# Kernel optimization log

Hardware: AMD Instinct MI355X
Metric: run time of the kernel (lower is better)

## Reference

```python
import jax, jax.numpy as jnp
import numpy as np

SPHERE_C = 128
M0 = 5            # m_size[0] = lmax+1
M_ALL = 19        # sum(m_size) for lmax=4, mmax=2
NUM_COEFF = 25    # (lmax+1)^2
RESCALE = 16.0
EPS = 1e-6        # flax LayerNorm default


def _layer_norm(h, g, b):
    mu = jnp.mean(h, axis=-1, keepdims=True)
    var = jnp.var(h, axis=-1, keepdims=True)
    return (h - mu) * jax.lax.rsqrt(var + EPS) * g + b


def setup_inputs() -> dict:
    key = jax.random.key(0)
    ks = jax.random.split(key, 16)
    n_nodes, n_edges = 6250, 100000
    inp = {
        'x': jax.random.normal(ks[0], (n_nodes, NUM_COEFF, SPHERE_C), jnp.float32),
        'x_edge': jax.random.normal(ks[1], (n_edges, 128), jnp.float32),
        'edge_index': jax.random.randint(ks[2], (2, n_edges), 0, n_nodes),
        'wigner_inv': jax.random.normal(ks[3], (n_edges, NUM_COEFF, M_ALL), jnp.float32),
        'edge_envelope': jax.random.uniform(ks[4], (n_edges, 1, 1), jnp.float32),
        'node_offset': 0,
    }
    # Radial MLP params: channels [128, 128, 128, M0*SPHERE_C=640]
    def lin(k, fan_in, fan_out):
        return jax.random.normal(k, (fan_in, fan_out), jnp.float32) / np.sqrt(fan_in).astype(np.float32)
    inp['W1'] = lin(ks[5], 128, 128); inp['b1'] = jnp.zeros((128,), jnp.float32)
    inp['g1'] = jnp.ones((128,), jnp.float32); inp['be1'] = jnp.zeros((128,), jnp.float32)
    inp['W2'] = lin(ks[6], 128, 128); inp['b2'] = jnp.zeros((128,), jnp.float32)
    inp['g2'] = jnp.ones((128,), jnp.float32); inp['be2'] = jnp.zeros((128,), jnp.float32)
    inp['W3'] = lin(ks[7], 128, M0 * SPHERE_C); inp['b3'] = jnp.zeros((M0 * SPHERE_C,), jnp.float32)
    return inp


def reference(x, x_edge, edge_index, wigner_inv, edge_envelope, node_offset,
              W1, b1, g1, be1, W2, b2, g2, be2, W3, b3):
    # Radial MLP: (Linear -> LayerNorm -> SiLU) x2 -> Linear
    h = jax.nn.silu(_layer_norm(x_edge @ W1 + b1, g1, be1))
    h = jax.nn.silu(_layer_norm(h @ W2 + b2, g2, be2))
    h = h @ W3 + b3                                      # [E, M0*C]
    x_edge_m_0 = h.reshape(-1, M0, SPHERE_C)             # [E, M0, C]
    # Embedding is zero for m>0 coefficients, so rotate only the first M0 columns
    # of wigner_inv: equivalent to padding to M_ALL then full einsum.
    emb = jnp.einsum('njk,nkc->njc', wigner_inv[:, :, :M0], x_edge_m_0)  # [E, 25, C]
    emb = emb * edge_envelope
    tgt = edge_index[1] - node_offset
    x_update = jax.ops.segment_sum(emb, tgt, num_segments=x.shape[0])
    return x + x_update / RESCALE
```

## Files before the change

kernel.cpp:

```cpp
#include <hip/hip_runtime.h>
#include <hip/hip_bf16.h>

typedef __attribute__((ext_vector_type(8))) short short8;
typedef __attribute__((ext_vector_type(4))) float floatx4;

static __device__ inline unsigned short f2bf(float f) {
    unsigned u = __float_as_uint(f);
    unsigned r = (u + 0x7fffu + ((u >> 16) & 1u)) >> 16;
    return (unsigned short)r;
}

__global__ __launch_bounds__(256) void mlp12_kernel(
    const float* __restrict__ xe,
    const float* __restrict__ W1, const float* __restrict__ b1,
    const float* __restrict__ g1, const float* __restrict__ be1,
    const float* __restrict__ W2, const float* __restrict__ b2,
    const float* __restrict__ g2, const float* __restrict__ be2,
    unsigned short* __restrict__ h2b, int E)
{
    __shared__ float As[64 * 132];
    __shared__ float Bs[16 * 128];
    __shared__ float redS[64 * 16];
    __shared__ float redQ[64 * 16];
    __shared__ float mrow[64];
    __shared__ float rrow[64];

    int t  = threadIdx.x;
    int tx = t & 15;
    int ty = t >> 4;
    int e0 = blockIdx.x * 64;

    for (int idx = t; idx < 64 * 32; idx += 256) {
        int row = idx >> 5;
        int c4  = (idx & 31) * 4;
        float4 v = make_float4(0.f, 0.f, 0.f, 0.f);
        if (e0 + row < E) v = *(const float4*)(xe + (size_t)(e0 + row) * 128 + c4);
        *(float4*)&As[row * 132 + c4] = v;
    }

    const float* Wl = W1; const float* bl = b1; const float* gl = g1; const float* bel = be1;
    float acc[4][8];

    for (int layer = 0; layer < 2; layer++) {
        for (int r = 0; r < 4; r++)
            for (int i = 0; i < 8; i++) acc[r][i] = 0.f;

        for (int kk = 0; kk < 128; kk += 16) {
            __syncthreads();
            for (int idx = t; idx < 16 * 32; idx += 256) {
                int row = idx >> 5;
                int c4  = (idx & 31) * 4;
                *(float4*)&Bs[row * 128 + c4] = *(const float4*)(Wl + (size_t)(kk + row) * 128 + c4);
            }
            __syncthreads();
            for (int k4 = 0; k4 < 16; k4 += 4) {
                float b[4][8];
                #pragma unroll
                for (int kb = 0; kb < 4; kb++) {
                    float4 bv0 = *(float4*)&Bs[(k4 + kb) * 128 + tx * 8];
                    float4 bv1 = *(float4*)&Bs[(k4 + kb) * 128 + tx * 8 + 4];
                    b[kb][0] = bv0.x; b[kb][1] = bv0.y; b[kb][2] = bv0.z; b[kb][3] = bv0.w;
                    b[kb][4] = bv1.x; b[kb][5] = bv1.y; b[kb][6] = bv1.z; b[kb][7] = bv1.w;
                }
                #pragma unroll
                for (int r = 0; r < 4; r++) {
                    float4 a4 = *(float4*)&As[(ty * 4 + r) * 132 + kk + k4];
                    #pragma unroll
                    for (int i = 0; i < 8; i++)
                        acc[r][i] += a4.x * b[0][i] + a4.y * b[1][i]
                                   + a4.z * b[2][i] + a4.w * b[3][i];
                }
            }
        }

        float gg[8], bebe[8];
        for (int i = 0; i < 8; i++) {
            float bb = bl[tx * 8 + i];
            gg[i]    = gl[tx * 8 + i];
            bebe[i]  = bel[tx * 8 + i];
            for (int r = 0; r < 4; r++) acc[r][i] += bb;
        }
        for (int r = 0; r < 4; r++) {
            float s = 0.f, q = 0.f;
            for (int i = 0; i < 8; i++) { s += acc[r][i]; q += acc[r][i] * acc[r][i]; }
            redS[(ty * 4 + r) * 16 + tx] = s;
            redQ[(ty * 4 + r) * 16 + tx] = q;
        }
        __syncthreads();
        if (t < 64) {
            float s = 0.f, q = 0.f;
            for (int i = 0; i < 16; i++) { s += redS[t * 16 + i]; q += redQ[t * 16 + i]; }
            float mu  = s * (1.f / 128.f);
            float var = q * (1.f / 128.f) - mu * mu;
            mrow[t] = mu;
            rrow[t] = rsqrtf(var + 1e-6f);
        }
        __syncthreads();
        for (int r = 0; r < 4; r++) {
            int e_loc = ty * 4 + r;
            float mu = mrow[e_loc], rs = rrow[e_loc];
            for (int i = 0; i < 8; i++) {
                float v = (acc[r][i] - mu) * rs * gg[i] + bebe[i];
                acc[r][i] = v / (1.f + __expf(-v));
            }
        }
        if (layer == 0) {
            for (int r = 0; r < 4; r++) {
                int e_loc = ty * 4 + r;
                for (int i = 0; i < 8; i++) As[e_loc * 132 + tx * 8 + i] = acc[r][i];
            }
            __syncthreads();
            Wl = W2; bl = b2; gl = g2; bel = be2;
        } else {
            for (int r = 0; r < 4; r++) {
                int e = e0 + ty * 4 + r;
                if (e < E) {
                    unsigned p[4];
                    for (int i = 0; i < 4; i++)
                        p[i] = (unsigned)f2bf(acc[r][2 * i]) | ((unsigned)f2bf(acc[r][2 * i + 1]) << 16);
                    *(uint4*)(h2b + (size_t)e * 128 + tx * 8) = make_uint4(p[0], p[1], p[2], p[3]);
                }
            }
        }
    }
}

__global__ __launch_bounds__(256) void w3t_kernel(const float* __restrict__ W3,
                                                  unsigned short* __restrict__ W3bT)
{
    int idx = blockIdx.x * 256 + threadIdx.x;
    int n = idx >> 7, k = idx & 127;
    W3bT[idx] = f2bf(W3[(size_t)k * 640 + n]);
}

__global__ __launch_bounds__(256) void gemm3_mfma_kernel(
    const unsigned short* __restrict__ h2b, const unsigned short* __restrict__ W3bT,
    const float* __restrict__ b3, unsigned short* __restrict__ h3b, int E)
{
    __shared__ unsigned short As[64 * 136];

    int t    = threadIdx.x;
    int lane = t & 63;
    int w    = t >> 6;
    int mw   = w & 1, nw = w >> 1;
    int l15  = lane & 15, quad = lane >> 4;
    int e0   = blockIdx.x * 64;
    int n0   = blockIdx.y * 128;

    for (int p = 0; p < 4; p++) {
        int idx = p * 256 + t;
        int row = idx >> 4;
        int c16 = idx & 15;
        uint4 v = make_uint4(0, 0, 0, 0);
        if (e0 + row < E) v = *(const uint4*)(h2b + (size_t)(e0 + row) * 128 + c16 * 8);
        *(uint4*)&As[row * 136 + c16 * 8] = v;
    }

    short8 bfrag[4][4];
    {
        const unsigned short* bbase = W3bT + (size_t)(n0 + nw * 64) * 128;
        for (int ks = 0; ks < 4; ks++)
            for (int nf = 0; nf < 4; nf++)
                bfrag[ks][nf] = *(const short8*)(bbase + (size_t)(nf * 16 + l15) * 128 + ks * 32 + quad * 8);
    }

    floatx4 acc[2][4];
    for (int mf = 0; mf < 2; mf++)
        for (int nf = 0; nf < 4; nf++)
            acc[mf][nf] = (floatx4){0.f, 0.f, 0.f, 0.f};

    __syncthreads();

    for (int ks = 0; ks < 4; ks++) {
        short8 afrag[2];
        for (int mf = 0; mf < 2; mf++)
            afrag[mf] = *(const short8*)&As[(mw * 32 + mf * 16 + l15) * 136 + ks * 32 + quad * 8];
        for (int mf = 0; mf < 2; mf++)
            for (int nf = 0; nf < 4; nf++)
                acc[mf][nf] = __builtin_amdgcn_mfma_f32_16x16x32_bf16(
                    bfrag[ks][nf], afrag[mf], acc[mf][nf], 0, 0, 0);
    }

    for (int nf = 0; nf < 4; nf++) {
        float4 bias = *(const float4*)&b3[n0 + nw * 64 + nf * 16 + quad * 4];
        for (int mf = 0; mf < 2; mf++) {
            int m = e0 + mw * 32 + mf * 16 + l15;
            if (m < E) {
                floatx4 v = acc[mf][nf];
                unsigned lo = (unsigned)f2bf(v[0] + bias.x) | ((unsigned)f2bf(v[1] + bias.y) << 16);
                unsigned hi = (unsigned)f2bf(v[2] + bias.z) | ((unsigned)f2bf(v[3] + bias.w) << 16);
                *(uint2*)(h3b + (size_t)m * 640 + n0 + nw * 64 + nf * 16 + quad * 4) = make_uint2(lo, hi);
            }
        }
    }
}

__global__ void hist_kernel(const int* __restrict__ ei, const int* __restrict__ noff,
                            int* __restrict__ counts, int E)
{
    int i = blockIdx.x * blockDim.x + threadIdx.x;
    if (i < E) {
        int tgt = ei[E + i] - noff[0];
        atomicAdd(&counts[tgt], 1);
    }
}

__global__ __launch_bounds__(1024) void scan_kernel(const int* __restrict__ counts,
                                                    int* __restrict__ offsets,
                                                    int* __restrict__ cursor, int N)
{
    __shared__ int part[1024];
    int t = threadIdx.x;
    int per = (N + 1023) / 1024;
    int beg = t * per;
    int end = beg + per; if (end > N) end = N; if (beg > N) beg = N;
    int s = 0;
    for (int i = beg; i < end; i++) s += counts[i];
    part[t] = s;
    __syncthreads();
    for (int off = 1; off < 1024; off <<= 1) {
        int v = part[t];
        int u = (t >= off) ? part[t - off] : 0;
        __syncthreads();
        part[t] = v + u;
        __syncthreads();
    }
    int run = (t == 0) ? 0 : part[t - 1];
    for (int i = beg; i < end; i++) {
        offsets[i] = run;
        cursor[i]  = run;
        run += counts[i];
    }
    if (t == 1023) offsets[N] = part[1023];
}

__global__ void scatter_kernel(const int* __restrict__ ei, const int* __restrict__ noff,
                               int* __restrict__ cursor, int* __restrict__ edge_ids, int E)
{
    int i = blockIdx.x * blockDim.x + threadIdx.x;
    if (i < E) {
        int tgt = ei[E + i] - noff[0];
        int pos = atomicAdd(&cursor[tgt], 1);
        edge_ids[pos] = i;
    }
}

__global__ __launch_bounds__(256) void gather_kernel(
    const float* __restrict__ x, const unsigned short* __restrict__ h3b,
    const float* __restrict__ wig, const float* __restrict__ env,
    const int* __restrict__ offsets, const int* __restrict__ edge_ids,
    float* __restrict__ out, int N)
{
    __shared__ float sw[2][25 * 8];
    __shared__ float sh[2][640];
    __shared__ float sev[2];
    int n = blockIdx.x;
    int t = threadIdx.x;
    int c = t & 127;
    int half = t >> 7;
    int njj = half ? 12 : 13;
    float acc[13];
    for (int i = 0; i < 13; i++) acc[i] = 0.f;

    int beg = offsets[n], end = offsets[n + 1];
    int wj = t / 5, wk = t - wj * 5;

    if (beg < end) {
        int e = edge_ids[beg];
        float wv = 0.f;
        if (t < 125) wv = wig[(size_t)e * 475 + wj * 19 + wk];
        const unsigned* hp = (const unsigned*)(h3b + (size_t)e * 640);
        unsigned h0 = hp[t];
        unsigned h1 = (t < 64) ? hp[256 + t] : 0u;
        float evv = (t == 0) ? env[e] : 0.f;
        if (t < 125) sw[0][wj * 8 + wk] = wv;
        sh[0][2 * t]     = __uint_as_float(h0 << 16);
        sh[0][2 * t + 1] = __uint_as_float(h0 & 0xffff0000u);
        if (t < 64) {
            sh[0][2 * (256 + t)]     = __uint_as_float(h1 << 16);
            sh[0][2 * (256 + t) + 1] = __uint_as_float(h1 & 0xffff0000u);
        }
        if (t == 0) sev[0] = evv;
    }
    __syncthreads();

    for (int ii = beg; ii < end; ii++) {
        int buf = (ii - beg) & 1;
        int nb  = buf ^ 1;
        bool has_next = (ii + 1 < end);
        float wv = 0.f, evv = 0.f;
        unsigned h0 = 0u, h1 = 0u;
        if (has_next) {
            int e_nxt = edge_ids[ii + 1];
            if (t < 125) wv = wig[(size_t)e_nxt * 475 + wj * 19 + wk];
            const unsigned* hp = (const unsigned*)(h3b + (size_t)e_nxt * 640);
            h0 = hp[t];
            if (t < 64) h1 = hp[256 + t];
            if (t == 0) evv = env[e_nxt];
        }

        float ev  = sev[buf];
        float hv0 = sh[buf][c],       hv1 = sh[buf][128 + c], hv2 = sh[buf][256 + c],
              hv3 = sh[buf][384 + c], hv4 = sh[buf][512 + c];
        for (int jj = 0; jj < njj; jj++) {
            int j = half + jj * 2;
            float4 w4 = *(float4*)&sw[buf][j * 8];
            float we  = sw[buf][j * 8 + 4];
            float d = w4.x * hv0 + w4.y * hv1 + w4.z * hv2 + w4.w * hv3 + we * hv4;
            acc[jj] += ev * d;
        }

        if (has_next) {
            if (t < 125) sw[nb][wj * 8 + wk] = wv;
            sh[nb][2 * t]     = __uint_as_float(h0 << 16);
            sh[nb][2 * t + 1] = __uint_as_float(h0 & 0xffff0000u);
            if (t < 64) {
                sh[nb][2 * (256 + t)]     = __uint_as_float(h1 << 16);
                sh[nb][2 * (256 + t) + 1] = __uint_as_float(h1 & 0xffff0000u);
            }
            if (t == 0) sev[nb] = evv;
        }
        __syncthreads();
    }

    size_t base = (size_t)n * 3200;
    for (int jj = 0; jj < njj; jj++) {
        int j = half + jj * 2;
        out[base + j * 128 + c] = x[base + j * 128 + c] + acc[jj] * 0.0625f;
    }
}

extern "C" void kernel_launch(void* const* d_in, const int* in_sizes, int n_in,
                              void* d_out, int out_size, void* d_ws, size_t ws_size,
                              hipStream_t stream) {
    const float* x          = (const float*)d_in[0];
    const float* x_edge     = (const float*)d_in[1];
    const int*   edge_index = (const int*)d_in[2];
    const float* wigner     = (const float*)d_in[3];
    const float* envel      = (const float*)d_in[4];
    const int*   node_off   = (const int*)d_in[5];
    const float* W1 = (const float*)d_in[6];
    const float* b1 = (const float*)d_in[7];
    const float* g1 = (const float*)d_in[8];
    const float* be1 = (const float*)d_in[9];
    const float* W2 = (const float*)d_in[10];
    const float* b2 = (const float*)d_in[11];
    const float* g2 = (const float*)d_in[12];
    const float* be2 = (const float*)d_in[13];
    const float* W3 = (const float*)d_in[14];
    const float* b3 = (const float*)d_in[15];
    float* out = (float*)d_out;

    int E = in_sizes[1] / 128;
    int N = in_sizes[0] / 3200;

    char* w = (char*)d_ws;
    unsigned short* h2b  = (unsigned short*)w; w += (size_t)E * 128 * sizeof(unsigned short);
    unsigned short* h3b  = (unsigned short*)w; w += (size_t)E * 640 * sizeof(unsigned short);
    unsigned short* W3bT = (unsigned short*)w; w += (size_t)640 * 128 * sizeof(unsigned short);
    int* counts   = (int*)w;            w += (size_t)((N + 63) & ~63) * sizeof(int);
    int* offsets  = (int*)w;            w += (size_t)((N + 1 + 63) & ~63) * sizeof(int);
    int* cursor   = (int*)w;            w += (size_t)((N + 63) & ~63) * sizeof(int);
    int* edge_ids = (int*)w;            w += (size_t)E * sizeof(int);

    hipMemsetAsync(counts, 0, (size_t)N * sizeof(int), stream);

    dim3 blk(256);
    mlp12_kernel<<<dim3((E + 63) / 64), blk, 0, stream>>>(
        x_edge, W1, b1, g1, be1, W2, b2, g2, be2, h2b, E);

    w3t_kernel<<<dim3(320), blk, 0, stream>>>(W3, W3bT);

    hist_kernel<<<dim3((E + 255) / 256), blk, 0, stream>>>(edge_index, node_off, counts, E);
    scan_kernel<<<dim3(1), dim3(1024), 0, stream>>>(counts, offsets, cursor, N);
    scatter_kernel<<<dim3((E + 255) / 256), blk, 0, stream>>>(edge_index, node_off, cursor, edge_ids, E);

    gemm3_mfma_kernel<<<dim3((E + 63) / 64, 5), blk, 0, stream>>>(h2b, W3bT, b3, h3b, E);

    gather_kernel<<<dim3(N), blk, 0, stream>>>(x, h3b, wigner, envel, offsets, edge_ids, out, N);
}
```

Before: 807.0 us.

## Run radial MLP layers 1-2 on bf16 MFMA with hi/lo split precision

```diff
diff --git a/kernel.cpp b/kernel.cpp
--- a/kernel.cpp
+++ b/kernel.cpp
@@ -10,115 +10,154 @@
     return (unsigned short)r;
 }
 
+static __device__ inline void split_bf(float f, unsigned short& hi, unsigned short& lo) {
+    unsigned u = __float_as_uint(f);
+    hi = (unsigned short)(u >> 16);
+    float hf = __uint_as_float(u & 0xffff0000u);
+    lo = f2bf(f - hf);
+}
+
+__global__ __launch_bounds__(256) void w12t_kernel(
+    const float* __restrict__ W1, const float* __restrict__ W2,
+    unsigned short* __restrict__ W1h, unsigned short* __restrict__ W1l,
+    unsigned short* __restrict__ W2h, unsigned short* __restrict__ W2l)
+{
+    int idx = blockIdx.x * 256 + threadIdx.x;
+    int which = idx >> 14;
+    int r = idx & 16383;
+    int n = r >> 7, k = r & 127;
+    const float* W = which ? W2 : W1;
+    float f = W[(size_t)k * 128 + n];
+    unsigned short hi, lo;
+    split_bf(f, hi, lo);
+    if (which) { W2h[r] = hi; W2l[r] = lo; }
+    else       { W1h[r] = hi; W1l[r] = lo; }
+}
+
 __global__ __launch_bounds__(256) void mlp12_kernel(
     const float* __restrict__ xe,
-    const float* __restrict__ W1, const float* __restrict__ b1,
-    const float* __restrict__ g1, const float* __restrict__ be1,
-    const float* __restrict__ W2, const float* __restrict__ b2,
-    const float* __restrict__ g2, const float* __restrict__ be2,
+    const unsigned short* __restrict__ W1h, const unsigned short* __restrict__ W1l,
+    const float* __restrict__ b1, const float* __restrict__ g1, const float* __restrict__ be1,
+    const unsigned short* __restrict__ W2h, const unsigned short* __restrict__ W2l,
+    const float* __restrict__ b2, const float* __restrict__ g2, const float* __restrict__ be2,
     unsigned short* __restrict__ h2b, int E)
 {
-    __shared__ float As[64 * 132];
-    __shared__ float Bs[16 * 128];
-    __shared__ float redS[64 * 16];
-    __shared__ float redQ[64 * 16];
-    __shared__ float mrow[64];
-    __shared__ float rrow[64];
-
-    int t  = threadIdx.x;
-    int tx = t & 15;
-    int ty = t >> 4;
-    int e0 = blockIdx.x * 64;
-
-    for (int idx = t; idx < 64 * 32; idx += 256) {
-        int row = idx >> 5;
-        int c4  = (idx & 31) * 4;
-        float4 v = make_float4(0.f, 0.f, 0.f, 0.f);
-        if (e0 + row < E) v = *(const float4*)(xe + (size_t)(e0 + row) * 128 + c4);
-        *(float4*)&As[row * 132 + c4] = v;
-    }
-
-    const float* Wl = W1; const float* bl = b1; const float* gl = g1; const float* bel = be1;
-    float acc[4][8];
-
+    __shared__ unsigned short Ah[64 * 136];
+    __shared__ unsigned short Al[64 * 136];
+
+    int t    = threadIdx.x;
+    int lane = t & 63;
+    int w    = t >> 6;
+    int l15  = lane & 15, quad = lane >> 4;
+    int row_loc = w * 16 + l15;
+    size_t e = (size_t)blockIdx.x * 64 + row_loc;
+    bool rowok = (e < (size_t)E);
+
+    floatx4 acc[8];
+
+    #pragma unroll
     for (int layer = 0; layer < 2; layer++) {
-        for (int r = 0; r < 4; r++)
-            for (int i = 0; i < 8; i++) acc[r][i] = 0.f;
-
-        for (int kk = 0; kk < 128; kk += 16) {
-            __syncthreads();
-            for (int idx = t; idx < 16 * 32; idx += 256) {
-                int row = idx >> 5;
-                int c4  = (idx & 31) * 4;
-                *(float4*)&Bs[row * 128 + c4] = *(const float4*)(Wl + (size_t)(kk + row) * 128 + c4);
-            }
-            __syncthreads();
-            for (int k4 = 0; k4 < 16; k4 += 4) {
-                float b[4][8];
-                #pragma unroll
-                for (int kb = 0; kb < 4; kb++) {
-                    float4 bv0 = *(float4*)&Bs[(k4 + kb) * 128 + tx * 8];
-                    float4 bv1 = *(float4*)&Bs[(k4 + kb) * 128 + tx * 8 + 4];
-                    b[kb][0] = bv0.x; b[kb][1] = bv0.y; b[kb][2] = bv0.z; b[kb][3] = bv0.w;
-                    b[kb][4] = bv1.x; b[kb][5] = bv1.y; b[kb][6] = bv1.z; b[kb][7] = bv1.w;
+        const unsigned short* Wh  = layer ? W2h : W1h;
+        const unsigned short* Wlo = layer ? W2l : W1l;
+        #pragma unroll
+        for (int nf = 0; nf < 8; nf++) acc[nf] = (floatx4){0.f, 0.f, 0.f, 0.f};
+
+        #pragma unroll
+        for (int ks = 0; ks < 4; ks++) {
+            short8 ah, al;
+            if (layer == 0) {
+                float f[8] = {0.f,0.f,0.f,0.f,0.f,0.f,0.f,0.f};
+                if (rowok) {
+                    float4 v0 = *(const float4*)(xe + e * 128 + ks * 32 + quad * 8);
+                    float4 v1 = *(const float4*)(xe + e * 128 + ks * 32 + quad * 8 + 4);
+                    f[0] = v0.x; f[1] = v0.y; f[2] = v0.z; f[3] = v0.w;
+                    f[4] = v1.x; f[5] = v1.y; f[6] = v1.z; f[7] = v1.w;
                 }
                 #pragma unroll
+                for (int j = 0; j < 8; j++) {
+                    unsigned short h, l;
+                    split_bf(f[j], h, l);
+                    ah[j] = (short)h; al[j] = (short)l;
+                }
+            } else {
+                ah = *(const short8*)&Ah[row_loc * 136 + ks * 32 + quad * 8];
+                al = *(const short8*)&Al[row_loc * 136 + ks * 32 + quad * 8];
+            }
+            #pragma unroll
+            for (int nf = 0; nf < 8; nf++) {
+                size_t wo = (size_t)(nf * 16 + l15) * 128 + ks * 32 + quad * 8;
+                short8 wh = *(const short8*)(Wh  + wo);
+                short8 wl = *(const short8*)(Wlo + wo);
+                acc[nf] = __builtin_amdgcn_mfma_f32_16x16x32_bf16(wh, ah, acc[nf], 0, 0, 0);
+                acc[nf] = __builtin_amdgcn_mfma_f32_16x16x32_bf16(wh, al, acc[nf], 0, 0, 0);
+                acc[nf] = __builtin_amdgcn_mfma_f32_16x16x32_bf16(wl, ah, acc[nf], 0, 0, 0);
+            }
+        }
+
+        const float* bl  = layer ? b2  : b1;
+        const float* gl  = layer ? g2  : g1;
+        const float* bel = layer ? be2 : be1;
+
+        float s = 0.f, q = 0.f;
+        #pragma unroll
+        for (int nf = 0; nf < 8; nf++) {
+            float4 bb = *(const float4*)(bl + nf * 16 + quad * 4);
+            acc[nf][0] += bb.x; acc[nf][1] += bb.y; acc[nf][2] += bb.z; acc[nf][3] += bb.w;
+            #pragma unroll
+            for (int r = 0; r < 4; r++) { s += acc[nf][r]; q += acc[nf][r] * acc[nf][r]; }
+        }
+        s += __shfl_xor(s, 16); s += __shfl_xor(s, 32);
+        q += __shfl_xor(q, 16); q += __shfl_xor(q, 32);
+        float mu  = s * (1.f / 128.f);
+        float var = q * (1.f / 128.f) - mu * mu;
+        float rs  = rsqrtf(var + 1e-6f);
+
+        if (layer == 0) {
+            #pragma unroll
+            for (int nf = 0; nf < 8; nf++) {
+                float4 gg  = *(const float4*)(gl  + nf * 16 + quad * 4);
+                float4 bb2 = *(const float4*)(bel + nf * 16 + quad * 4);
+                float vv[4];
+                vv[0] = (acc[nf][0] - mu) * rs * gg.x + bb2.x;
+                vv[1] = (acc[nf][1] - mu) * rs * gg.y + bb2.y;
+                vv[2] = (acc[nf][2] - mu) * rs * gg.z + bb2.z;
+                vv[3] = (acc[nf][3] - mu) * rs * gg.w + bb2.w;
+                unsigned short h4[4], l4[4];
+                #pragma unroll
                 for (int r = 0; r < 4; r++) {
-                    float4 a4 = *(float4*)&As[(ty * 4 + r) * 132 + kk + k4];
+                    float v = vv[r];
+                    v = v / (1.f + __expf(-v));
+                    split_bf(v, h4[r], l4[r]);
+                }
+                *(uint2*)&Ah[row_loc * 136 + nf * 16 + quad * 4] =
+                    make_uint2((unsigned)h4[0] | ((unsigned)h4[1] << 16),
+                               (unsigned)h4[2] | ((unsigned)h4[3] << 16));
+                *(uint2*)&Al[row_loc * 136 + nf * 16 + quad * 4] =
+                    make_uint2((unsigned)l4[0] | ((unsigned)l4[1] << 16),
+                               (unsigned)l4[2] | ((unsigned)l4[3] << 16));
+            }
+            __syncthreads();
+        } else {
+            if (rowok) {
+                #pragma unroll
+                for (int nf = 0; nf < 8; nf++) {
+                    float4 gg  = *(const float4*)(gl  + nf * 16 + quad * 4);
+                    float4 bb2 = *(const float4*)(bel + nf * 16 + quad * 4);
+                    unsigned short p[4];
+                    float vv[4];
+                    vv[0] = (acc[nf][0] - mu) * rs * gg.x + bb2.x;
+                    vv[1] = (acc[nf][1] - mu) * rs * gg.y + bb2.y;
+                    vv[2] = (acc[nf][2] - mu) * rs * gg.z + bb2.z;
+                    vv[3] = (acc[nf][3] - mu) * rs * gg.w + bb2.w;
                     #pragma unroll
-                    for (int i = 0; i < 8; i++)
-                        acc[r][i] += a4.x * b[0][i] + a4.y * b[1][i]
-                                   + a4.z * b[2][i] + a4.w * b[3][i];
-                }
-            }
-        }
-
-        float gg[8], bebe[8];
-        for (int i = 0; i < 8; i++) {
-            float bb = bl[tx * 8 + i];
-            gg[i]    = gl[tx * 8 + i];
-            bebe[i]  = bel[tx * 8 + i];
-            for (int r = 0; r < 4; r++) acc[r][i] += bb;
-        }
-        for (int r = 0; r < 4; r++) {
-            float s = 0.f, q = 0.f;
-            for (int i = 0; i < 8; i++) { s += acc[r][i]; q += acc[r][i] * acc[r][i]; }
-            redS[(ty * 4 + r) * 16 + tx] = s;
-            redQ[(ty * 4 + r) * 16 + tx] = q;
-        }
-        __syncthreads();
-        if (t < 64) {
-            float s = 0.f, q = 0.f;
-            for (int i = 0; i < 16; i++) { s += redS[t * 16 + i]; q += redQ[t * 16 + i]; }
-            float mu  = s * (1.f / 128.f);
-            float var = q * (1.f / 128.f) - mu * mu;
-            mrow[t] = mu;
-            rrow[t] = rsqrtf(var + 1e-6f);
-        }
-        __syncthreads();
-        for (int r = 0; r < 4; r++) {
-            int e_loc = ty * 4 + r;
-            float mu = mrow[e_loc], rs = rrow[e_loc];
-            for (int i = 0; i < 8; i++) {
-                float v = (acc[r][i] - mu) * rs * gg[i] + bebe[i];
-                acc[r][i] = v / (1.f + __expf(-v));
-            }
-        }
-        if (layer == 0) {
-            for (int r = 0; r < 4; r++) {
-                int e_loc = ty * 4 + r;
-                for (int i = 0; i < 8; i++) As[e_loc * 132 + tx * 8 + i] = acc[r][i];
-            }
-            __syncthreads();
-            Wl = W2; bl = b2; gl = g2; bel = be2;
-        } else {
-            for (int r = 0; r < 4; r++) {
-                int e = e0 + ty * 4 + r;
-                if (e < E) {
-                    unsigned p[4];
-                    for (int i = 0; i < 4; i++)
-                        p[i] = (unsigned)f2bf(acc[r][2 * i]) | ((unsigned)f2bf(acc[r][2 * i + 1]) << 16);
-                    *(uint4*)(h2b + (size_t)e * 128 + tx * 8) = make_uint4(p[0], p[1], p[2], p[3]);
+                    for (int r = 0; r < 4; r++) {
+                        float v = vv[r];
+                        v = v / (1.f + __expf(-v));
+                        p[r] = f2bf(v);
+                    }
+                    *(uint2*)(h2b + e * 128 + nf * 16 + quad * 4) =
+                        make_uint2((unsigned)p[0] | ((unsigned)p[1] << 16),
+                                   (unsigned)p[2] | ((unsigned)p[3] << 16));
                 }
             }
         }
@@ -358,6 +397,10 @@
     unsigned short* h2b  = (unsigned short*)w; w += (size_t)E * 128 * sizeof(unsigned short);
     unsigned short* h3b  = (unsigned short*)w; w += (size_t)E * 640 * sizeof(unsigned short);
     unsigned short* W3bT = (unsigned short*)w; w += (size_t)640 * 128 * sizeof(unsigned short);
+    unsigned short* W1h  = (unsigned short*)w; w += (size_t)128 * 128 * sizeof(unsigned short);
+    unsigned short* W1l  = (unsigned short*)w; w += (size_t)128 * 128 * sizeof(unsigned short);
+    unsigned short* W2h  = (unsigned short*)w; w += (size_t)128 * 128 * sizeof(unsigned short);
+    unsigned short* W2l  = (unsigned short*)w; w += (size_t)128 * 128 * sizeof(unsigned short);
     int* counts   = (int*)w;            w += (size_t)((N + 63) & ~63) * sizeof(int);
     int* offsets  = (int*)w;            w += (size_t)((N + 1 + 63) & ~63) * sizeof(int);
     int* cursor   = (int*)w;            w += (size_t)((N + 63) & ~63) * sizeof(int);
@@ -366,8 +409,10 @@
     hipMemsetAsync(counts, 0, (size_t)N * sizeof(int), stream);
 
     dim3 blk(256);
+    w12t_kernel<<<dim3(128), blk, 0, stream>>>(W1, W2, W1h, W1l, W2h, W2l);
+
     mlp12_kernel<<<dim3((E + 63) / 64), blk, 0, stream>>>(
-        x_edge, W1, b1, g1, be1, W2, b2, g2, be2, h2b, E);
+        x_edge, W1h, W1l, b1, g1, be1, W2h, W2l, b2, g2, be2, h2b, E);
 
     w3t_kernel<<<dim3(320), blk, 0, stream>>>(W3, W3bT);
 
```

Measured after the change: 701.1 us. 13.1% less time.
